# Kernel optimization log

Measured on AMD Instinct MI355X. Metric: run time of the kernel, lower is better.

Reference implementation:

```python
import jax, jax.numpy as jnp
import numpy as np

DIM = 1024
HEADS = 16
DIM_HEAD = 64
INNER = HEADS * DIM_HEAD  # 1024
EPS = 1e-5


def layer_norm(x, g, b):
    mu = jnp.mean(x, axis=-1, keepdims=True)
    var = jnp.var(x, axis=-1, keepdims=True)
    return (x - mu) * jax.lax.rsqrt(var + EPS) * g + b


def setup_inputs() -> dict:
    key = jax.random.key(0)
    ks = jax.random.split(key, 8)
    s = 0.02
    return {
        "x": jax.random.normal(ks[0], (2, 2048, DIM), dtype=jnp.float32),
        "w_qkv": jax.random.normal(ks[1], (DIM, 3 * INNER), dtype=jnp.float32) * s,
        "w_out": jax.random.normal(ks[2], (INNER, DIM), dtype=jnp.float32) * s,
        "b_out": jnp.zeros((DIM,), jnp.float32),
        "g1": jnp.ones((DIM,), jnp.float32),
        "bt1": jnp.zeros((DIM,), jnp.float32),
        "g2": jnp.ones((DIM,), jnp.float32),
        "bt2": jnp.zeros((DIM,), jnp.float32),
        "w1": jax.random.normal(ks[3], (DIM, DIM), dtype=jnp.float32) * s,  # ff hidden = dim_out = DIM
        "b1": jnp.zeros((DIM,), jnp.float32),
        "w2": jax.random.normal(ks[4], (DIM, DIM), dtype=jnp.float32) * s,
        "b2": jnp.zeros((DIM,), jnp.float32),
    }


def reference(x, w_qkv, w_out, b_out, g1, bt1, g2, bt2, w1, b1, w2, b2):
    b, n, _ = x.shape
    scale = DIM_HEAD ** (-0.5)
    x_in = x
    xl = layer_norm(x, g1, bt1)
    qkv = xl @ w_qkv  # [b, n, 3*inner]
    q, k, v = jnp.split(qkv, 3, axis=-1)
    def split_heads(t):
        return t.reshape(b, n, HEADS, DIM_HEAD).transpose(0, 2, 1, 3)  # b h n d
    q, k, v = map(split_heads, (q, k, v))
    dots = jnp.einsum('bhid,bhjd->bhij', q, k) * scale
    attn = jax.nn.softmax(dots, axis=-1)
    out = jnp.einsum('bhij,bhjd->bhid', attn, v)
    out = out.transpose(0, 2, 1, 3).reshape(b, n, INNER)
    out = out @ w_out + b_out
    out = out + x_in
    h = layer_norm(out, g2, bt2)
    h = jax.nn.gelu(h @ w1 + b1, approximate=False) @ w2 + b2
    return h + out
```

## Files before the change

kernel.cpp:

```cpp
#include <hip/hip_runtime.h>
#include <math.h>

typedef __attribute__((ext_vector_type(4))) float f32x4;
typedef __attribute__((ext_vector_type(8))) short bf16x8;
typedef __attribute__((ext_vector_type(8))) unsigned short u16x8;

#define DIM 1024
#define SEQ 2048
#define NHEADS 16
#define DH 64

__device__ __forceinline__ unsigned short f2bf(float f) {
    unsigned int u = __builtin_bit_cast(unsigned int, f);
    u += 0x7fffu + ((u >> 16) & 1u);
    return (unsigned short)(u >> 16);
}

__device__ __forceinline__ float bf2f(unsigned short s) {
    unsigned int u = (unsigned int)s << 16;
    return __builtin_bit_cast(float, u);
}

__device__ __forceinline__ unsigned int cvt_pk_bf16(float lo, float hi) {
    unsigned int r;
    asm("v_cvt_pk_bf16_f32 %0, %1, %2" : "=v"(r) : "v"(lo), "v"(hi));
    return r;
}

__device__ __forceinline__ float fexp2(float x) {
    float r;
    asm("v_exp_f32 %0, %1" : "=v"(r) : "v"(x));
    return r;
}

__device__ __forceinline__ void gld16(const unsigned short* g, unsigned short* l) {
    __builtin_amdgcn_global_load_lds((const __attribute__((address_space(1))) void*)g,
                                     (__attribute__((address_space(3))) void*)l, 16, 0, 0);
}

__global__ __launch_bounds__(256) void wtrans_ln(const float* __restrict__ wq,
                                                 const float* __restrict__ wo,
                                                 const float* __restrict__ wf1,
                                                 const float* __restrict__ wf2,
                                                 unsigned short* __restrict__ oq,
                                                 unsigned short* __restrict__ oo,
                                                 unsigned short* __restrict__ of1,
                                                 unsigned short* __restrict__ of2, float sc,
                                                 const float* __restrict__ x,
                                                 const float* __restrict__ g1,
                                                 const float* __restrict__ bt1,
                                                 unsigned short* __restrict__ xl) {
    int z = blockIdx.z;
    int bxi = blockIdx.x;
    int tid = threadIdx.x;
    if (z == 4) {
        int row = blockIdx.y * 128 + bxi;
        const float4* xr = (const float4*)(x + (size_t)row * DIM);
        float4 v = xr[tid];
        float s1 = v.x + v.y + v.z + v.w;
        float s2 = v.x * v.x + v.y * v.y + v.z * v.z + v.w * v.w;
#pragma unroll
        for (int m = 32; m >= 1; m >>= 1) {
            s1 += __shfl_xor(s1, m);
            s2 += __shfl_xor(s2, m);
        }
        __shared__ float r1[4], r2[4];
        int w = tid >> 6;
        if ((tid & 63) == 0) { r1[w] = s1; r2[w] = s2; }
        __syncthreads();
        s1 = r1[0] + r1[1] + r1[2] + r1[3];
        s2 = r2[0] + r2[1] + r2[2] + r2[3];
        float mu = s1 * (1.0f / DIM);
        float var = s2 * (1.0f / DIM) - mu * mu;
        float rstd = rsqrtf(var + 1e-5f);
        float4 g4 = ((const float4*)g1)[tid];
        float4 b4 = ((const float4*)bt1)[tid];
        ushort4 ov;
        ov.x = f2bf((v.x - mu) * rstd * g4.x + b4.x);
        ov.y = f2bf((v.y - mu) * rstd * g4.y + b4.y);
        ov.z = f2bf((v.z - mu) * rstd * g4.z + b4.z);
        ov.w = f2bf((v.w - mu) * rstd * g4.w + b4.w);
        *(ushort4*)(xl + (size_t)row * DIM + tid * 4) = ov;
        return;
    }
    if (bxi >= (z == 0 ? 96 : 32)) return;
    const float* w = z == 0 ? wq : z == 1 ? wo : z == 2 ? wf1 : wf2;
    unsigned short* wt = z == 0 ? oq : z == 1 ? oo : z == 2 ? of1 : of2;
    int N = z == 0 ? 3072 : 1024;
    int scale_n = z == 0 ? 1024 : 0;
    const int K = 1024;
    __shared__ float t[32][33];
    int n0 = bxi * 32, k0 = blockIdx.y * 32;
    int c = tid & 31, rb = tid >> 5;
#pragma unroll
    for (int i = 0; i < 4; ++i) {
        int r = rb + i * 8;
        t[r][c] = w[(size_t)(k0 + r) * N + n0 + c];
    }
    __syncthreads();
#pragma unroll
    for (int i = 0; i < 4; ++i) {
        int r = rb + i * 8;
        float v = t[c][r];
        if (n0 + r < scale_n) v *= sc;
        wt[(size_t)(n0 + r) * K + k0 + c] = f2bf(v);
    }
}

__global__ __launch_bounds__(256) void ln_kernel(const float* __restrict__ x,
                                                 const float* __restrict__ g,
                                                 const float* __restrict__ bt,
                                                 unsigned short* __restrict__ o) {
    int row = blockIdx.x, tid = threadIdx.x;
    const float4* xr = (const float4*)(x + (size_t)row * DIM);
    float4 v = xr[tid];
    float s1 = v.x + v.y + v.z + v.w;
    float s2 = v.x * v.x + v.y * v.y + v.z * v.z + v.w * v.w;
#pragma unroll
    for (int m = 32; m >= 1; m >>= 1) {
        s1 += __shfl_xor(s1, m);
        s2 += __shfl_xor(s2, m);
    }
    __shared__ float r1[4], r2[4];
    int w = tid >> 6;
    if ((tid & 63) == 0) { r1[w] = s1; r2[w] = s2; }
    __syncthreads();
    s1 = r1[0] + r1[1] + r1[2] + r1[3];
    s2 = r2[0] + r2[1] + r2[2] + r2[3];
    float mu = s1 * (1.0f / DIM);
    float var = s2 * (1.0f / DIM) - mu * mu;
    float rstd = rsqrtf(var + 1e-5f);
    float4 g4 = ((const float4*)g)[tid];
    float4 b4 = ((const float4*)bt)[tid];
    ushort4 ov;
    ov.x = f2bf((v.x - mu) * rstd * g4.x + b4.x);
    ov.y = f2bf((v.y - mu) * rstd * g4.y + b4.y);
    ov.z = f2bf((v.z - mu) * rstd * g4.z + b4.z);
    ov.w = f2bf((v.w - mu) * rstd * g4.w + b4.w);
    *(ushort4*)(o + (size_t)row * DIM + tid * 4) = ov;
}

template <int BN, int BK, int OBF, int BIAS, int GELU_, int RESID, int VT>
__global__ __launch_bounds__(256) void gemm_kernel(const unsigned short* __restrict__ A,
                                                   const unsigned short* __restrict__ BT,
                                                   void* __restrict__ C,
                                                   const float* __restrict__ bias,
                                                   const float* __restrict__ resid,
                                                   unsigned short* __restrict__ vt,
                                                   int M, int N, int K, int nbx) {
    constexpr int U = BK / 8;
    constexpr int NAU = 128 * U;
    constexpr int NBU = BN * U;
    constexpr int PT = (NAU + NBU) / 256;
    constexpr int NJ = BN / 32;
    constexpr int KK = BK / 32;
    extern __shared__ char smem[];
    unsigned short* As = (unsigned short*)smem;
    unsigned short* Bs = As + 3 * 128 * BK;
    int tid = threadIdx.x;
    int lane = tid & 63, w = tid >> 6;
    int l15 = lane & 15, lhi = lane >> 4;
    int nwg = gridDim.x, wg = blockIdx.x;
    int swz = (wg & 7) * (nwg >> 3) + (wg >> 3);
    int bx = swz % nbx, by = swz / nbx;
    int row0 = by * 128, col0 = bx * BN;
    int wrow = (w >> 1) * 64, wcol = (w & 1) * (16 * NJ);
    f32x4 zero = {0.f, 0.f, 0.f, 0.f};
    f32x4 acc[4][NJ];
#pragma unroll
    for (int i = 0; i < 4; ++i)
#pragma unroll
        for (int j = 0; j < NJ; ++j) acc[i][j] = zero;
    auto stage = [&](int buf, int kt) {
#pragma unroll
        for (int p = 0; p < PT; ++p) {
            if (p * 256 < NAU) {
                int u = tid + p * 256;
                int r = u / U, cu = u % U;
                int scu = cu ^ (r & (U - 1));
                gld16(A + (size_t)(row0 + r) * K + kt * BK + scu * 8, As + buf * 128 * BK + u * 8);
            } else {
                int ub = tid + p * 256 - NAU;
                int r = ub / U, cu = ub % U;
                int scu = cu ^ (r & (U - 1));
                gld16(BT + (size_t)(col0 + r) * K + kt * BK + scu * 8, Bs + buf * BN * BK + ub * 8);
            }
        }
    };
    int nk = K / BK;
    stage(0, 0);
    stage(1, 1);
    asm volatile("s_waitcnt vmcnt(%0)" ::"i"(PT) : "memory");
    __builtin_amdgcn_s_barrier();
    __builtin_amdgcn_sched_barrier(0);
    int cur = 0;
    for (int kt = 0; kt < nk; ++kt) {
        int nxt2 = cur + 2 >= 3 ? cur - 1 : cur + 2;
        if (kt + 2 < nk) stage(nxt2, kt + 2);
        const unsigned short* Ab = As + cur * 128 * BK;
        const unsigned short* Bb = Bs + cur * BN * BK;
        bf16x8 af[4][KK], bfr[NJ][KK];
#pragma unroll
        for (int i = 0; i < 4; ++i)
#pragma unroll
            for (int kk = 0; kk < KK; ++kk) {
                int rr = wrow + i * 16 + l15;
                int up = (kk * 4 + lhi) ^ (rr & (U - 1));
                af[i][kk] = *(const bf16x8*)&Ab[rr * BK + up * 8];
            }
#pragma unroll
        for (int j = 0; j < NJ; ++j)
#pragma unroll
            for (int kk = 0; kk < KK; ++kk) {
                int rr = wcol + j * 16 + l15;
                int up = (kk * 4 + lhi) ^ (rr & (U - 1));
                bfr[j][kk] = *(const bf16x8*)&Bb[rr * BK + up * 8];
            }
#pragma unroll
        for (int kk = 0; kk < KK; ++kk)
#pragma unroll
            for (int i = 0; i < 4; ++i)
#pragma unroll
                for (int j = 0; j < NJ; ++j)
                    acc[i][j] = __builtin_amdgcn_mfma_f32_16x16x32_bf16(af[i][kk], bfr[j][kk],
                                                                        acc[i][j], 0, 0, 0);
        __builtin_amdgcn_sched_barrier(0);
        if (kt + 1 < nk) {
            if (kt + 2 < nk)
                asm volatile("s_waitcnt vmcnt(%0)" ::"i"(PT) : "memory");
            else
                asm volatile("s_waitcnt vmcnt(0)" ::: "memory");
            __builtin_amdgcn_s_barrier();
            __builtin_amdgcn_sched_barrier(0);
        }
        cur = cur + 1 == 3 ? 0 : cur + 1;
    }
    if (VT && col0 >= 2048) {
        __syncthreads();
        unsigned short* Ct = (unsigned short*)smem;
#pragma unroll
        for (int i = 0; i < 4; ++i)
#pragma unroll
            for (int j = 0; j < NJ; ++j)
#pragma unroll
                for (int r = 0; r < 4; ++r)
                    Ct[(wrow + i * 16 + lhi * 4 + r) * 130 + (wcol + j * 16 + l15)] =
                        f2bf(acc[i][j][r]);
        __syncthreads();
        int l = tid & 63, wv = tid >> 6;
        int sig = (l & 32) | ((l & 4) << 2) | ((l & 24) >> 1) | (l & 3);
        int b = row0 >> 11, n0 = row0 & 2047;
        int h0 = (col0 - 2048) >> 6;
        for (int c = wv * 64; c < wv * 64 + 64; ++c) {
            int ntl = c & 1, hl = (c >> 1) & 1, d = c >> 2;
            unsigned short v = Ct[(ntl * 64 + sig) * 130 + hl * 64 + d];
            vt[((size_t)(b * NHEADS + h0 + hl) * DH + d) * SEQ + n0 + ntl * 64 + l] = v;
        }
        return;
    }
#pragma unroll
    for (int i = 0; i < 4; ++i)
#pragma unroll
        for (int j = 0; j < NJ; ++j)
#pragma unroll
            for (int r = 0; r < 4; ++r) {
                int row = row0 + wrow + i * 16 + lhi * 4 + r;
                int col = col0 + wcol + j * 16 + l15;
                float v = acc[i][j][r];
                if (BIAS) v += bias[col];
                if (GELU_) v = 0.5f * v * (1.0f + erff(v * 0.70710678118f));
                if (RESID) v += resid[(size_t)row * N + col];
                if (OBF)
                    ((unsigned short*)C)[(size_t)row * N + col] = f2bf(v);
                else
                    ((float*)C)[(size_t)row * N + col] = v;
            }
}

__global__ __launch_bounds__(256) void attn_kernel(const unsigned short* __restrict__ qkv,
                                                   const unsigned short* __restrict__ vt,
                                                   unsigned short* __restrict__ po,
                                                   float* __restrict__ pl) {
    __shared__ unsigned short Ks[64 * 64];
    __shared__ unsigned short Vs[64 * 64];
    int tid = threadIdx.x;
    int lane = tid & 63, w = tid >> 6;
    int l15 = lane & 15, lhi = lane >> 4;
    int wg = blockIdx.x;
    int swz = (wg & 7) * 128 + (wg >> 3);
    int qt = swz & 15, half = (swz >> 4) & 1, h = (swz >> 5) & 15, b = swz >> 9;
    bf16x8 qf[2][2];
#pragma unroll
    for (int qg = 0; qg < 2; ++qg) {
        const unsigned short* qb =
            qkv + (size_t)(b * SEQ + qt * 128 + w * 32 + qg * 16 + l15) * 3072 + h * DH;
        qf[qg][0] = *(const bf16x8*)(qb + lhi * 8);
        qf[qg][1] = *(const bf16x8*)(qb + 32 + lhi * 8);
    }
    f32x4 zero = {0.f, 0.f, 0.f, 0.f};
    f32x4 oacc[2][4], lacc[2];
#pragma unroll
    for (int qg = 0; qg < 2; ++qg) {
        lacc[qg] = zero;
#pragma unroll
        for (int i = 0; i < 4; ++i) oacc[qg][i] = zero;
    }
    const short one_s = (short)0x3F80;
    bf16x8 ones = {one_s, one_s, one_s, one_s, one_s, one_s, one_s, one_s};
    int srow = tid >> 3;
    int scx = (tid & 7) ^ (srow & 7);
    const unsigned short* kb = qkv + (size_t)b * SEQ * 3072 + 1024 + h * DH;
    const unsigned short* vb = vt + (size_t)(b * NHEADS + h) * DH * SEQ;
    const unsigned short* k0 = kb + (size_t)srow * 3072 + scx * 8;
    const unsigned short* v0 = vb + (size_t)srow * SEQ + scx * 8;
    auto stage = [&](int kg) {
        unsigned short* lk = &Ks[0] + tid * 8;
        unsigned short* lv = &Vs[0] + tid * 8;
        gld16(k0 + (size_t)kg * 64 * 3072, lk);
        gld16(k0 + ((size_t)kg * 64 + 32) * 3072, lk + 2048);
        gld16(v0 + kg * 64, lv);
        gld16(v0 + (size_t)32 * SEQ + kg * 64, lv + 2048);
    };
    int kx = l15 & 7;
    const int NT2 = SEQ / 64 / 2;
    for (int kt = 0; kt < NT2; ++kt) {
        stage(half * NT2 + kt);
        asm volatile("s_waitcnt vmcnt(0)" ::: "memory");
        __builtin_amdgcn_s_barrier();
        __builtin_amdgcn_sched_barrier(0);
        f32x4 sacc[2][4];
#pragma unroll
        for (int nt = 0; nt < 4; ++nt) {
            bf16x8 kf0 = *(const bf16x8*)&Ks[(nt * 16 + l15) * 64 + ((lhi ^ kx) * 8)];
            bf16x8 kf1 = *(const bf16x8*)&Ks[(nt * 16 + l15) * 64 + (((4 + lhi) ^ kx) * 8)];
#pragma unroll
            for (int qg = 0; qg < 2; ++qg) {
                f32x4 z = __builtin_amdgcn_mfma_f32_16x16x32_bf16(kf0, qf[qg][0], zero, 0, 0, 0);
                sacc[qg][nt] = __builtin_amdgcn_mfma_f32_16x16x32_bf16(kf1, qf[qg][1], z, 0, 0, 0);
            }
        }
        bf16x8 pf[2][2];
#pragma unroll
        for (int qg = 0; qg < 2; ++qg)
#pragma unroll
            for (int kc = 0; kc < 2; ++kc) {
                union { bf16x8 v; unsigned int u[4]; } pu;
                pu.u[0] = cvt_pk_bf16(fexp2(sacc[qg][2 * kc][0]), fexp2(sacc[qg][2 * kc][1]));
                pu.u[1] = cvt_pk_bf16(fexp2(sacc[qg][2 * kc][2]), fexp2(sacc[qg][2 * kc][3]));
                pu.u[2] = cvt_pk_bf16(fexp2(sacc[qg][2 * kc + 1][0]), fexp2(sacc[qg][2 * kc + 1][1]));
                pu.u[3] = cvt_pk_bf16(fexp2(sacc[qg][2 * kc + 1][2]), fexp2(sacc[qg][2 * kc + 1][3]));
                pf[qg][kc] = pu.v;
            }
#pragma unroll
        for (int dt = 0; dt < 4; ++dt)
#pragma unroll
            for (int kc = 0; kc < 2; ++kc) {
                bf16x8 vf = *(const bf16x8*)&Vs[(dt * 16 + l15) * 64 + (((kc * 4 + lhi) ^ kx) * 8)];
#pragma unroll
                for (int qg = 0; qg < 2; ++qg)
                    oacc[qg][dt] =
                        __builtin_amdgcn_mfma_f32_16x16x32_bf16(vf, pf[qg][kc], oacc[qg][dt], 0, 0, 0);
            }
#pragma unroll
        for (int qg = 0; qg < 2; ++qg) {
            lacc[qg] = __builtin_amdgcn_mfma_f32_16x16x32_bf16(ones, pf[qg][0], lacc[qg], 0, 0, 0);
            lacc[qg] = __builtin_amdgcn_mfma_f32_16x16x32_bf16(ones, pf[qg][1], lacc[qg], 0, 0, 0);
        }
        __builtin_amdgcn_sched_barrier(0);
        if (kt + 1 < NT2) {
            __builtin_amdgcn_s_barrier();
            __builtin_amdgcn_sched_barrier(0);
        }
    }
#pragma unroll
    for (int qg = 0; qg < 2; ++qg) {
        int rrow = b * SEQ + qt * 128 + w * 32 + qg * 16 + l15;
        unsigned short* pob = po + ((size_t)half * 4096 + rrow) * DIM + h * DH;
#pragma unroll
        for (int dt = 0; dt < 4; ++dt) {
            ushort4 st;
            st.x = f2bf(oacc[qg][dt][0]);
            st.y = f2bf(oacc[qg][dt][1]);
            st.z = f2bf(oacc[qg][dt][2]);
            st.w = f2bf(oacc[qg][dt][3]);
            *(ushort4*)(pob + dt * 16 + lhi * 4) = st;
        }
        if (lhi == 0) pl[((size_t)half * 4096 + rrow) * NHEADS + h] = lacc[qg][0];
    }
}

__global__ __launch_bounds__(256) void attn_combine(const unsigned short* __restrict__ po,
                                                    const float* __restrict__ pl,
                                                    unsigned short* __restrict__ o) {
    int r = blockIdx.x, tid = threadIdx.x;
    int d0 = tid * 4, h = d0 >> 6;
    ushort4 a = *(const ushort4*)(po + (size_t)r * DIM + d0);
    ushort4 c = *(const ushort4*)(po + (size_t)(4096 + r) * DIM + d0);
    float rl = 1.0f / (pl[(size_t)r * NHEADS + h] + pl[(size_t)(4096 + r) * NHEADS + h]);
    ushort4 ov;
    ov.x = f2bf((bf2f(a.x) + bf2f(c.x)) * rl);
    ov.y = f2bf((bf2f(a.y) + bf2f(c.y)) * rl);
    ov.z = f2bf((bf2f(a.z) + bf2f(c.z)) * rl);
    ov.w = f2bf((bf2f(a.w) + bf2f(c.w)) * rl);
    *(ushort4*)(o + (size_t)r * DIM + d0) = ov;
}

extern "C" void kernel_launch(void* const* d_in, const int* in_sizes, int n_in,
                              void* d_out, int out_size, void* d_ws, size_t ws_size,
                              hipStream_t stream) {
    (void)in_sizes; (void)n_in; (void)out_size; (void)ws_size;
    const float* x = (const float*)d_in[0];
    const float* w_qkv = (const float*)d_in[1];
    const float* w_out = (const float*)d_in[2];
    const float* b_out = (const float*)d_in[3];
    const float* g1 = (const float*)d_in[4];
    const float* bt1 = (const float*)d_in[5];
    const float* g2 = (const float*)d_in[6];
    const float* bt2 = (const float*)d_in[7];
    const float* w1 = (const float*)d_in[8];
    const float* b1 = (const float*)d_in[9];
    const float* w2 = (const float*)d_in[10];
    const float* b2 = (const float*)d_in[11];
    float* out = (float*)d_out;

    char* ws = (char*)d_ws;
    size_t off = 0;
    auto alloc = [&](size_t bytes) {
        void* p = ws + off;
        off += (bytes + 255) & ~(size_t)255;
        return p;
    };
    const int R = 2 * SEQ;
    unsigned short* xl    = (unsigned short*)alloc((size_t)R * DIM * 2);
    unsigned short* wqkvT = (unsigned short*)alloc((size_t)3 * DIM * DIM * 2);
    unsigned short* woutT = (unsigned short*)alloc((size_t)DIM * DIM * 2);
    unsigned short* w1T   = (unsigned short*)alloc((size_t)DIM * DIM * 2);
    unsigned short* w2T   = (unsigned short*)alloc((size_t)DIM * DIM * 2);
    unsigned short* qkvb  = (unsigned short*)alloc((size_t)R * 3 * DIM * 2);
    unsigned short* vtb   = (unsigned short*)alloc((size_t)R * DIM * 2);
    unsigned short* attO  = (unsigned short*)alloc((size_t)R * DIM * 2);
    unsigned short* h2    = (unsigned short*)alloc((size_t)R * DIM * 2);
    unsigned short* ffn1  = (unsigned short*)alloc((size_t)R * DIM * 2);
    unsigned short* po = (unsigned short*)alloc((size_t)2 * R * DIM * 2);
    float* pl = (float*)alloc((size_t)2 * R * NHEADS * 4);

    const float CS = 0.125f * 1.44269504f;
    wtrans_ln<<<dim3(128, 32, 5), 256, 0, stream>>>(w_qkv, w_out, w1, w2, wqkvT, woutT, w1T, w2T,
                                                    CS, x, g1, bt1, xl);

    const unsigned int SH_QKV = (3 * 128 * 32 + 3 * 128 * 32) * 2;
    const unsigned int SH_FFN = (3 * 128 * 64 + 3 * 64 * 64) * 2;
    gemm_kernel<128, 32, 1, 0, 0, 0, 1>
        <<<dim3((3 * DIM / 128) * (R / 128)), 256, SH_QKV, stream>>>(
            xl, wqkvT, qkvb, nullptr, nullptr, vtb, R, 3 * DIM, DIM, 3 * DIM / 128);
    attn_kernel<<<2 * NHEADS * (SEQ / 128) * 2, 256, 0, stream>>>(qkvb, vtb, po, pl);
    attn_combine<<<R, 256, 0, stream>>>(po, pl, attO);
    gemm_kernel<64, 64, 0, 1, 0, 1, 0><<<dim3((DIM / 64) * (R / 128)), 256, SH_FFN, stream>>>(
        attO, woutT, out, b_out, x, nullptr, R, DIM, DIM, DIM / 64);
    ln_kernel<<<R, 256, 0, stream>>>(out, g2, bt2, h2);
    gemm_kernel<64, 64, 1, 1, 1, 0, 0><<<dim3((DIM / 64) * (R / 128)), 256, SH_FFN, stream>>>(
        h2, w1T, ffn1, b1, nullptr, nullptr, R, DIM, DIM, DIM / 64);
    gemm_kernel<64, 64, 0, 1, 0, 1, 0><<<dim3((DIM / 64) * (R / 128)), 256, SH_FFN, stream>>>(
        ffn1, w2T, out, b2, out, nullptr, R, DIM, DIM, DIM / 64);
}
```

Measured before the change: 168.3 us.

## Fuse attention split-combine into out-projection GEMM and keep residual in bf16

Removes the separate attn_combine kernel. A new out-projection GEMM loads both partial attention outputs and their softmax denominators, normalizes them in registers, and writes the result to shared memory as its A operand. The post-attention residual stream is now stored in bf16, so the second layernorm and the final FFN residual read half as many bytes. It also raises wave priority around the attention MFMA section. In exchange, the residual loses precision from being rounded to bf16, and the new GEMM issues twice the A-side global loads and runs a register-staged pipeline.

```diff
diff --git a/kernel.cpp b/kernel.cpp
--- a/kernel.cpp
+++ b/kernel.cpp
@@ -107,15 +107,15 @@
     }
 }
 
-__global__ __launch_bounds__(256) void ln_kernel(const float* __restrict__ x,
-                                                 const float* __restrict__ g,
-                                                 const float* __restrict__ bt,
-                                                 unsigned short* __restrict__ o) {
+__global__ __launch_bounds__(256) void ln_bf16(const unsigned short* __restrict__ x,
+                                               const float* __restrict__ g,
+                                               const float* __restrict__ bt,
+                                               unsigned short* __restrict__ o) {
     int row = blockIdx.x, tid = threadIdx.x;
-    const float4* xr = (const float4*)(x + (size_t)row * DIM);
-    float4 v = xr[tid];
-    float s1 = v.x + v.y + v.z + v.w;
-    float s2 = v.x * v.x + v.y * v.y + v.z * v.z + v.w * v.w;
+    ushort4 v4 = *(const ushort4*)(x + (size_t)row * DIM + tid * 4);
+    float vx = bf2f(v4.x), vy = bf2f(v4.y), vz = bf2f(v4.z), vw = bf2f(v4.w);
+    float s1 = vx + vy + vz + vw;
+    float s2 = vx * vx + vy * vy + vz * vz + vw * vw;
 #pragma unroll
     for (int m = 32; m >= 1; m >>= 1) {
         s1 += __shfl_xor(s1, m);
@@ -133,10 +133,10 @@
     float4 g4 = ((const float4*)g)[tid];
     float4 b4 = ((const float4*)bt)[tid];
     ushort4 ov;
-    ov.x = f2bf((v.x - mu) * rstd * g4.x + b4.x);
-    ov.y = f2bf((v.y - mu) * rstd * g4.y + b4.y);
-    ov.z = f2bf((v.z - mu) * rstd * g4.z + b4.z);
-    ov.w = f2bf((v.w - mu) * rstd * g4.w + b4.w);
+    ov.x = f2bf((vx - mu) * rstd * g4.x + b4.x);
+    ov.y = f2bf((vy - mu) * rstd * g4.y + b4.y);
+    ov.z = f2bf((vz - mu) * rstd * g4.z + b4.z);
+    ov.w = f2bf((vw - mu) * rstd * g4.w + b4.w);
     *(ushort4*)(o + (size_t)row * DIM + tid * 4) = ov;
 }
 
@@ -145,7 +145,7 @@
                                                    const unsigned short* __restrict__ BT,
                                                    void* __restrict__ C,
                                                    const float* __restrict__ bias,
-                                                   const float* __restrict__ resid,
+                                                   const void* __restrict__ resid,
                                                    unsigned short* __restrict__ vt,
                                                    int M, int N, int K, int nbx) {
     constexpr int U = BK / 8;
@@ -269,11 +269,141 @@
                 float v = acc[i][j][r];
                 if (BIAS) v += bias[col];
                 if (GELU_) v = 0.5f * v * (1.0f + erff(v * 0.70710678118f));
-                if (RESID) v += resid[(size_t)row * N + col];
+                if (RESID == 1) v += ((const float*)resid)[(size_t)row * N + col];
+                if (RESID == 2) v += bf2f(((const unsigned short*)resid)[(size_t)row * N + col]);
                 if (OBF)
                     ((unsigned short*)C)[(size_t)row * N + col] = f2bf(v);
                 else
                     ((float*)C)[(size_t)row * N + col] = v;
+            }
+}
+
+__global__ __launch_bounds__(256) void gemm_oproj(const unsigned short* __restrict__ po,
+                                                  const float* __restrict__ pl,
+                                                  const unsigned short* __restrict__ BT,
+                                                  unsigned short* __restrict__ outb,
+                                                  const float* __restrict__ bias,
+                                                  const float* __restrict__ xres) {
+    constexpr int BK = 64, BN = 64, U = 8, NJ = 2, KK = 2, nk = 16;
+    __shared__ unsigned short As[2][128 * 64];
+    __shared__ unsigned short Bs[2][64 * 64];
+    int tid = threadIdx.x;
+    int lane = tid & 63, w = tid >> 6;
+    int l15 = lane & 15, lhi = lane >> 4;
+    int nwg = gridDim.x, wg = blockIdx.x;
+    int swz = (wg & 7) * (nwg >> 3) + (wg >> 3);
+    int bx = swz % 16, by = swz / 16;
+    int row0 = by * 128, col0 = bx * BN;
+    int wrow = (w >> 1) * 64, wcol = (w & 1) * 32;
+    f32x4 zero = {0.f, 0.f, 0.f, 0.f};
+    f32x4 acc[4][NJ];
+#pragma unroll
+    for (int i = 0; i < 4; ++i)
+#pragma unroll
+        for (int j = 0; j < NJ; ++j) acc[i][j] = zero;
+    uint4 a0[4], a1[4];
+    float pl0[4], pl1[4];
+    auto issueA = [&](int kt) {
+#pragma unroll
+        for (int p = 0; p < 4; ++p) {
+            int u = tid + p * 256;
+            int r = u >> 3, cu = u & 7;
+            int scu = cu ^ (r & 7);
+            size_t rrow = row0 + r;
+            a0[p] = *(const uint4*)(po + rrow * DIM + kt * 64 + scu * 8);
+            a1[p] = *(const uint4*)(po + (4096 + rrow) * DIM + kt * 64 + scu * 8);
+            pl0[p] = pl[rrow * NHEADS + kt];
+            pl1[p] = pl[(4096 + rrow) * NHEADS + kt];
+        }
+    };
+    auto writeA = [&](int buf) {
+#pragma unroll
+        for (int p = 0; p < 4; ++p) {
+            int u = tid + p * 256;
+            float rl = 1.0f / (pl0[p] + pl1[p]);
+            const unsigned short* e0 = (const unsigned short*)&a0[p];
+            const unsigned short* e1 = (const unsigned short*)&a1[p];
+            uint4 pk;
+            unsigned int* pku = (unsigned int*)&pk;
+#pragma unroll
+            for (int j = 0; j < 4; ++j) {
+                float lo = (bf2f(e0[2 * j]) + bf2f(e1[2 * j])) * rl;
+                float hi = (bf2f(e0[2 * j + 1]) + bf2f(e1[2 * j + 1])) * rl;
+                pku[j] = cvt_pk_bf16(lo, hi);
+            }
+            *(uint4*)(&As[buf][0] + u * 8) = pk;
+        }
+    };
+    auto stageB = [&](int buf, int kt) {
+#pragma unroll
+        for (int p = 0; p < 2; ++p) {
+            int ub = tid + p * 256;
+            int r = ub >> 3, cu = ub & 7;
+            int scu = cu ^ (r & 7);
+            gld16(BT + (size_t)(col0 + r) * DIM + kt * 64 + scu * 8, &Bs[buf][0] + ub * 8);
+        }
+    };
+    issueA(0);
+    stageB(0, 0);
+    asm volatile("s_waitcnt vmcnt(0)" ::: "memory");
+    writeA(0);
+    issueA(1);
+    stageB(1, 1);
+    asm volatile("s_waitcnt lgkmcnt(0)" ::: "memory");
+    __builtin_amdgcn_s_barrier();
+    __builtin_amdgcn_sched_barrier(0);
+    for (int kt = 0; kt < nk; ++kt) {
+        int cur = kt & 1;
+        const unsigned short* Ab = &As[cur][0];
+        const unsigned short* Bb = &Bs[cur][0];
+        bf16x8 af[4][KK], bfr[NJ][KK];
+#pragma unroll
+        for (int i = 0; i < 4; ++i)
+#pragma unroll
+            for (int kk = 0; kk < KK; ++kk) {
+                int rr = wrow + i * 16 + l15;
+                int up = (kk * 4 + lhi) ^ (rr & 7);
+                af[i][kk] = *(const bf16x8*)&Ab[rr * BK + up * 8];
+            }
+#pragma unroll
+        for (int j = 0; j < NJ; ++j)
+#pragma unroll
+            for (int kk = 0; kk < KK; ++kk) {
+                int rr = wcol + j * 16 + l15;
+                int up = (kk * 4 + lhi) ^ (rr & 7);
+                bfr[j][kk] = *(const bf16x8*)&Bb[rr * BK + up * 8];
+            }
+#pragma unroll
+        for (int kk = 0; kk < KK; ++kk)
+#pragma unroll
+            for (int i = 0; i < 4; ++i)
+#pragma unroll
+                for (int j = 0; j < NJ; ++j)
+                    acc[i][j] = __builtin_amdgcn_mfma_f32_16x16x32_bf16(af[i][kk], bfr[j][kk],
+                                                                        acc[i][j], 0, 0, 0);
+        __builtin_amdgcn_sched_barrier(0);
+        if (kt + 1 < nk) {
+            asm volatile("s_waitcnt vmcnt(0)" ::: "memory");
+            writeA(cur ^ 1);
+            asm volatile("s_waitcnt lgkmcnt(0)" ::: "memory");
+            __builtin_amdgcn_s_barrier();
+            __builtin_amdgcn_sched_barrier(0);
+            if (kt + 2 < nk) {
+                issueA(kt + 2);
+                stageB(cur, kt + 2);
+            }
+        }
+    }
+#pragma unroll
+    for (int i = 0; i < 4; ++i)
+#pragma unroll
+        for (int j = 0; j < NJ; ++j)
+#pragma unroll
+            for (int r = 0; r < 4; ++r) {
+                int row = row0 + wrow + i * 16 + lhi * 4 + r;
+                int col = col0 + wcol + j * 16 + l15;
+                float v = acc[i][j][r] + bias[col] + xres[(size_t)row * DIM + col];
+                outb[(size_t)row * DIM + col] = f2bf(v);
             }
 }
 
@@ -328,6 +458,7 @@
         asm volatile("s_waitcnt vmcnt(0)" ::: "memory");
         __builtin_amdgcn_s_barrier();
         __builtin_amdgcn_sched_barrier(0);
+        __builtin_amdgcn_s_setprio(1);
         f32x4 sacc[2][4];
 #pragma unroll
         for (int nt = 0; nt < 4; ++nt) {
@@ -366,6 +497,7 @@
             lacc[qg] = __builtin_amdgcn_mfma_f32_16x16x32_bf16(ones, pf[qg][0], lacc[qg], 0, 0, 0);
             lacc[qg] = __builtin_amdgcn_mfma_f32_16x16x32_bf16(ones, pf[qg][1], lacc[qg], 0, 0, 0);
         }
+        __builtin_amdgcn_s_setprio(0);
         __builtin_amdgcn_sched_barrier(0);
         if (kt + 1 < NT2) {
             __builtin_amdgcn_s_barrier();
@@ -387,22 +519,6 @@
         }
         if (lhi == 0) pl[((size_t)half * 4096 + rrow) * NHEADS + h] = lacc[qg][0];
     }
-}
-
-__global__ __launch_bounds__(256) void attn_combine(const unsigned short* __restrict__ po,
-                                                    const float* __restrict__ pl,
-                                                    unsigned short* __restrict__ o) {
-    int r = blockIdx.x, tid = threadIdx.x;
-    int d0 = tid * 4, h = d0 >> 6;
-    ushort4 a = *(const ushort4*)(po + (size_t)r * DIM + d0);
-    ushort4 c = *(const ushort4*)(po + (size_t)(4096 + r) * DIM + d0);
-    float rl = 1.0f / (pl[(size_t)r * NHEADS + h] + pl[(size_t)(4096 + r) * NHEADS + h]);
-    ushort4 ov;
-    ov.x = f2bf((bf2f(a.x) + bf2f(c.x)) * rl);
-    ov.y = f2bf((bf2f(a.y) + bf2f(c.y)) * rl);
-    ov.z = f2bf((bf2f(a.z) + bf2f(c.z)) * rl);
-    ov.w = f2bf((bf2f(a.w) + bf2f(c.w)) * rl);
-    *(ushort4*)(o + (size_t)r * DIM + d0) = ov;
 }
 
 extern "C" void kernel_launch(void* const* d_in, const int* in_sizes, int n_in,
@@ -438,7 +554,7 @@
     unsigned short* w2T   = (unsigned short*)alloc((size_t)DIM * DIM * 2);
     unsigned short* qkvb  = (unsigned short*)alloc((size_t)R * 3 * DIM * 2);
     unsigned short* vtb   = (unsigned short*)alloc((size_t)R * DIM * 2);
-    unsigned short* attO  = (unsigned short*)alloc((size_t)R * DIM * 2);
+    unsigned short* outb  = (unsigned short*)alloc((size_t)R * DIM * 2);
     unsigned short* h2    = (unsigned short*)alloc((size_t)R * DIM * 2);
     unsigned short* ffn1  = (unsigned short*)alloc((size_t)R * DIM * 2);
     unsigned short* po = (unsigned short*)alloc((size_t)2 * R * DIM * 2);
@@ -454,12 +570,10 @@
         <<<dim3((3 * DIM / 128) * (R / 128)), 256, SH_QKV, stream>>>(
             xl, wqkvT, qkvb, nullptr, nullptr, vtb, R, 3 * DIM, DIM, 3 * DIM / 128);
     attn_kernel<<<2 * NHEADS * (SEQ / 128) * 2, 256, 0, stream>>>(qkvb, vtb, po, pl);
-    attn_combine<<<R, 256, 0, stream>>>(po, pl, attO);
-    gemm_kernel<64, 64, 0, 1, 0, 1, 0><<<dim3((DIM / 64) * (R / 128)), 256, SH_FFN, stream>>>(
-        attO, woutT, out, b_out, x, nullptr, R, DIM, DIM, DIM / 64);
-    ln_kernel<<<R, 256, 0, stream>>>(out, g2, bt2, h2);
+    gemm_oproj<<<dim3((DIM / 64) * (R / 128)), 256, 0, stream>>>(po, pl, woutT, outb, b_out, x);
+    ln_bf16<<<R, 256, 0, stream>>>(outb, g2, bt2, h2);
     gemm_kernel<64, 64, 1, 1, 1, 0, 0><<<dim3((DIM / 64) * (R / 128)), 256, SH_FFN, stream>>>(
         h2, w1T, ffn1, b1, nullptr, nullptr, R, DIM, DIM, DIM / 64);
-    gemm_kernel<64, 64, 0, 1, 0, 1, 0><<<dim3((DIM / 64) * (R / 128)), 256, SH_FFN, stream>>>(
-        ffn1, w2T, out, b2, out, nullptr, R, DIM, DIM, DIM / 64);
-}
+    gemm_kernel<64, 64, 0, 1, 0, 2, 0><<<dim3((DIM / 64) * (R / 128)), 256, SH_FFN, stream>>>(
+        ffn1, w2T, out, b2, outb, nullptr, R, DIM, DIM, DIM / 64);
+}
```

Result: slower. 176.7 us (+5.0%).
